# Kernel optimization log

Measured on AMD Instinct MI355X. Metric: run time of the kernel, lower is better.

Reference implementation:

```python
import jax, jax.numpy as jnp
import numpy as np

HID = 128          # hidden_channels
NG = 256           # number of graphs in batch
NL = 50000         # ligand nodes
NP = 150000        # protein nodes
E = 500000         # edges (ligand->protein); rev edges are the reverse
RBF_COUNT = 8
D_MAX = 5.0


def _rbf(d):
    # d: [E] distances -> [E, 8] gaussian RBF expansion (D_min=0, D_max=5, count=8)
    mu = jnp.linspace(0.0, D_MAX, RBF_COUNT)
    sigma = D_MAX / RBF_COUNT
    return jnp.exp(-(((d[:, None] - mu[None, :]) / sigma) ** 2))


def setup_inputs() -> dict:
    key = jax.random.key(0)
    ks = jax.random.split(key, 24)
    s = 0.05
    inp = {
        "x_ligand": jax.random.normal(ks[0], (NL, 44), jnp.float32),
        "x_protein": jax.random.normal(ks[1], (NP, 44), jnp.float32),
        "edge_attr": jax.random.uniform(ks[2], (E, 1), jnp.float32) * D_MAX,
        "edge_src": jax.random.randint(ks[3], (E,), 0, NL),
        "edge_dst": jax.random.randint(ks[4], (E,), 0, NP),
        "ligand_batch": jnp.sort(jax.random.randint(ks[5], (NL,), 0, NG)),
        # shared node embedding and edge embedding
        "W_node": jax.random.normal(ks[6], (44, HID), jnp.float32) * s,
        "W_el": jax.random.normal(ks[7], (1, 8), jnp.float32) * s,
        # 6 NConvs: index = layer*2 + (0: ligand->protein, 1: protein->ligand)
        "Wb": jax.random.normal(ks[8], (6, RBF_COUNT, HID), jnp.float32) * s,
        "bb": jnp.zeros((6, HID), jnp.float32),
        "Wn": jax.random.normal(ks[9], (6, HID, HID), jnp.float32) * s,
        "Ws": jax.random.normal(ks[10], (6, HID, HID), jnp.float32) * s,
        "bconv": jnp.zeros((6, HID), jnp.float32),
        # edge MLP: [2*HID+8 -> 512 -> 128] (BN in eval mode = identity, dropout off)
        "W1": jax.random.normal(ks[11], (2 * HID + 8, 512), jnp.float32) * s,
        "b1": jnp.zeros((512,), jnp.float32),
        "W2": jax.random.normal(ks[12], (512, 128), jnp.float32) * s,
        "b2": jnp.zeros((128,), jnp.float32),
        # lin_mpl: 128 -> out_channels//2 = 128
        "Wm": jax.random.normal(ks[13], (128, 128), jnp.float32) * s,
        "bm": jnp.zeros((128,), jnp.float32),
    }
    return inp


def _nconv(x_src, x_dst, src, dst, n_dst, rbf_feat, Wb_i, bb_i, Wn_i, Ws_i, b_i):
    # base = SiLU(Linear(rbf)); message = fc_neigh(base * x_j); aggr = mean over dst
    base = jax.nn.silu(rbf_feat @ Wb_i + bb_i)              # [E, HID]
    msg = (base * x_src[src]) @ Wn_i                         # gather + mul + GEMM
    agg = jax.ops.segment_sum(msg, dst, num_segments=n_dst)  # [n_dst, HID]
    deg = jax.ops.segment_sum(jnp.ones((src.shape[0], 1), msg.dtype), dst,
                              num_segments=n_dst)
    agg = agg / jnp.maximum(deg, 1.0)
    return x_dst @ Ws_i + agg + b_i


def reference(x_ligand, x_protein, edge_attr, edge_src, edge_dst, ligand_batch,
              W_node, W_el, Wb, bb, Wn, Ws, bconv, W1, b1, W2, b2, Wm, bm):
    lrelu = lambda v: jax.nn.leaky_relu(v, 0.01)
    xl = x_ligand @ W_node   # [NL, HID]
    xp = x_protein @ W_node  # [NP, HID]
    rbf_feat = _rbf(jnp.squeeze(edge_attr, -1))  # [E, 8]

    xl_sum = jnp.zeros_like(xl)
    xp_sum = jnp.zeros_like(xp)
    for l in range(3):
        i_lp, i_pl = 2 * l, 2 * l + 1
        # HeteroConv applies both edge types to the SAME input dict
        xp_new = lrelu(_nconv(xl, xp, edge_src, edge_dst, NP, rbf_feat,
                              Wb[i_lp], bb[i_lp], Wn[i_lp], Ws[i_lp], bconv[i_lp]))
        xl_new = lrelu(_nconv(xp, xl, edge_dst, edge_src, NL, rbf_feat,
                              Wb[i_pl], bb[i_pl], Wn[i_pl], Ws[i_pl], bconv[i_pl]))
        xl, xp = xl_new, xp_new
        xl_sum = xl_sum + xl
        xp_sum = xp_sum + xp

    # edge readout on the ligand->protein edges
    edge_repr = jnp.concatenate([xl_sum[edge_src], xp_sum[edge_dst]], axis=-1)
    d_pl = edge_attr @ W_el                                   # [E, 8]
    edge_repr = jnp.concatenate([edge_repr, d_pl], axis=1)    # [E, 2*HID+8]
    # edge_mlp (eval mode: BatchNorm identity, dropout off)
    m_pl = jax.nn.relu(edge_repr @ W1 + b1) @ W2 + b2         # [E, 128]
    w_pl = jnp.tanh(m_pl @ Wm + bm)                           # [E, 128]
    edge_batch = ligand_batch[edge_src]
    m_w = jax.ops.segment_sum(w_pl * m_pl, edge_batch, num_segments=NG)
    m_max = jax.ops.segment_max(m_pl, edge_batch, num_segments=NG)
    m_max = jnp.where(jnp.isfinite(m_max), m_max, 0.0)        # empty segments -> 0
    return jnp.concatenate([m_w, m_max], axis=1)              # [NG, 256]
```

## Files before the change

kernel.cpp:

```cpp
#include <hip/hip_runtime.h>
#include <hip/hip_bf16.h>


#define NLn 50000
#define NPn 150000
#define En  500000
#define NBL 1563
#define NBP 4688

typedef __attribute__((ext_vector_type(8))) short short8;
typedef __attribute__((ext_vector_type(4))) float float4v;

__device__ __forceinline__ float bf2f(unsigned short u){ return __uint_as_float(((unsigned)u) << 16); }
__device__ __forceinline__ float bflo(unsigned u){ return __uint_as_float(u << 16); }
__device__ __forceinline__ float bfhi(unsigned u){ return __uint_as_float(u & 0xffff0000u); }
__device__ __forceinline__ unsigned short f2bf(float f){
  __hip_bfloat16 h = __float2bfloat16(f);
  return *reinterpret_cast<unsigned short*>(&h);
}
__device__ __forceinline__ unsigned encf(float f){
  unsigned u = __float_as_uint(f);
  return (u & 0x80000000u) ? ~u : (u | 0x80000000u);
}
__device__ __forceinline__ float tanh_fast(float x){
  return 1.f - 2.f/(__expf(2.f*x) + 1.f);
}

__global__ __launch_bounds__(256) void k_embed(
    const float* __restrict__ Xl, const float* __restrict__ Xp,
    const float* __restrict__ Wnode,
    unsigned short* __restrict__ xl0, unsigned short* __restrict__ xp0){
  __shared__ float xs[1408];
  int b = blockIdx.x, tid = threadIdx.x;
  bool isL = b < NBL;
  const float* X = isL ? Xl : Xp;
  unsigned short* out = isL ? xl0 : xp0;
  int n = isL ? NLn : NPn;
  int n0 = (isL ? b : b - NBL) * 32;
  int nrows = n - n0; if (nrows > 32) nrows = 32;
  int nflt = nrows * 44;
  const float4* Xv = (const float4*)(X + (size_t)n0*44);
  for (int j = tid; j*4 < nflt; j += 256){
    float4 v = Xv[j];
    xs[j*4+0]=v.x; xs[j*4+1]=v.y; xs[j*4+2]=v.z; xs[j*4+3]=v.w;
  }
  __syncthreads();
  int c = tid & 127, half = tid >> 7;
  float acc[16];
  #pragma unroll
  for (int r=0;r<16;r++) acc[r]=0.f;
  const float* xrow = xs + half*16*44;
  #pragma unroll 4
  for (int k=0;k<44;k++){
    float w = Wnode[k*128 + c];
    #pragma unroll
    for (int r=0;r<16;r++) acc[r] += xrow[r*44 + k] * w;
  }
  int rbase = n0 + half*16;
  #pragma unroll
  for (int r=0;r<16;r++){
    int nn = rbase + r;
    if (nn < n) out[(size_t)nn*128 + c] = f2bf(acc[r]);
  }
}

__global__ __launch_bounds__(256) void k_prep(
    unsigned* __restrict__ cntz, unsigned* __restrict__ mmaxz, unsigned* __restrict__ outz,
    const float* __restrict__ Wel, const float* __restrict__ W1, float* __restrict__ vvec,
    const float* __restrict__ W2, unsigned short* __restrict__ w2t,
    const float* __restrict__ Wm, unsigned short* __restrict__ wmt,
    const float* __restrict__ Ws, const float* __restrict__ Wn,
    unsigned short* __restrict__ wcat, unsigned short* __restrict__ w1t,
    const float* __restrict__ Wb, const float* __restrict__ bb,
    unsigned short* __restrict__ lut){
  __shared__ float gw[16];
  int b = blockIdx.x, tid = threadIdx.x;
  if (b < 196){
    for (long i = (long)b*256 + tid; i < 200000; i += 196*256) cntz[i] = 0u;
  } else if (b < 324){
    mmaxz[(b-196)*256 + tid] = 0u;
  } else if (b < 580){
    outz[(b-324)*256 + tid] = 0u;
  } else if (b < 582){
    int j = (b-580)*256 + tid;
    float s = 0.f;
    #pragma unroll
    for (int r=0;r<8;r++) s += Wel[r]*W1[(256+r)*512 + j];
    vvec[j] = s;
  } else if (b < 838){
    int gid = (b-582)*256 + tid;
    int n = gid >> 9, k = gid & 511;
    w2t[n*512 + k] = f2bf(W2[k*128 + n]);
  } else if (b < 902){
    int gid = (b-838)*256 + tid;
    int n = gid >> 7, k = gid & 127;
    wmt[n*128 + k] = f2bf(Wm[k*128 + n]);
  } else if (b < 1670){
    int gid = (b-902)*256 + tid;
    int i = gid >> 15, rem = gid & 32767;
    int n = rem >> 8, k = rem & 255;
    float v = (k < 128) ? Ws[i*16384 + k*128 + n] : Wn[i*16384 + (k-128)*128 + n];
    wcat[gid] = f2bf(v);
  } else if (b < 2182){
    int gid = (b-1670)*256 + tid;
    int part = gid >> 16, rem = gid & 65535;
    int n = rem >> 7, k = rem & 127;
    w1t[gid] = f2bf(W1[(part*128 + k)*512 + n]);
  } else {
    int gid0 = (b-2182)*256;
    int c = tid & 127, half = tid >> 7;
    int bin0 = (gid0 >> 7) & 4095;
    int i = gid0 >> 19;
    if (tid < 16){
      int bn = bin0 + (tid >> 3), j = tid & 7;
      float d = ((float)bn + 0.5f) * 0.001220703125f;
      float a = (d - 0.7142857143f*(float)j) * 1.6f;
      gw[tid] = __expf(-a*a);
    }
    __syncthreads();
    float s = bb[i*128 + c];
    const float* g = gw + half*8;
    #pragma unroll
    for (int j=0;j<8;j++) s += g[j] * Wb[i*1024 + j*128 + c];
    lut[gid0 + tid] = f2bf(s / (1.f + __expf(-s)));
  }
}

__global__ __launch_bounds__(256) void k_count(const int* __restrict__ esrc,
    const int* __restrict__ edst, unsigned* __restrict__ cntL, unsigned* __restrict__ cntP){
  int e = blockIdx.x*256 + threadIdx.x;
  if (e >= En) return;
  atomicAdd(&cntL[esrc[e]], 1u);
  atomicAdd(&cntP[edst[e]], 1u);
}
__global__ __launch_bounds__(256) void k_cs2(const unsigned* __restrict__ cntL,
    unsigned* __restrict__ rowptrL, unsigned* __restrict__ bsumL,
    const unsigned* __restrict__ cntP, unsigned* __restrict__ rowptrP,
    unsigned* __restrict__ bsumP){
  bool isL = blockIdx.x < 49;
  const unsigned* cnt = isL ? cntL : cntP;
  unsigned* rowptr = isL ? rowptrL : rowptrP;
  unsigned* bsum = isL ? bsumL : bsumP;
  int n = isL ? NLn : NPn;
  int lb = isL ? blockIdx.x : blockIdx.x - 49;
  __shared__ unsigned ts[256];
  int tid = threadIdx.x;
  int base = lb*1024 + tid*4;
  unsigned v[4], run = 0;
  #pragma unroll
  for (int j=0;j<4;j++){ v[j] = run; run += (base+j < n) ? cnt[base+j] : 0u; }
  ts[tid] = run; __syncthreads();
  for (int off=1; off<256; off<<=1){
    unsigned t = (tid>=off) ? ts[tid-off] : 0u; __syncthreads();
    ts[tid] += t; __syncthreads();
  }
  unsigned excl = ts[tid] - run;
  #pragma unroll
  for (int j=0;j<4;j++) if (base+j < n) rowptr[base+j] = excl + v[j];
  if (tid == 255) bsum[lb] = ts[255];
}
__global__ void k_sb2(unsigned* __restrict__ bsumL, unsigned* __restrict__ bsumP){
  unsigned* bsum = blockIdx.x ? bsumP : bsumL;
  int nc = blockIdx.x ? 147 : 49;
  __shared__ unsigned ts[256];
  int tid = threadIdx.x;
  unsigned x = (tid < nc) ? bsum[tid] : 0u;
  ts[tid] = x; __syncthreads();
  for (int off=1; off<256; off<<=1){
    unsigned t = (tid>=off) ? ts[tid-off] : 0u; __syncthreads();
    ts[tid] += t; __syncthreads();
  }
  if (tid < nc) bsum[tid] = ts[tid] - x;
}
__global__ __launch_bounds__(256) void k_ao2(
    unsigned* __restrict__ rowptrL, unsigned* __restrict__ cursorL,
    const unsigned* __restrict__ bsumL,
    unsigned* __restrict__ rowptrP, unsigned* __restrict__ cursorP,
    const unsigned* __restrict__ bsumP){
  bool isL = blockIdx.x < 196;
  unsigned* rowptr = isL ? rowptrL : rowptrP;
  unsigned* cursor = isL ? cursorL : cursorP;
  const unsigned* bsum = isL ? bsumL : bsumP;
  int n = isL ? NLn : NPn;
  int i = (isL ? blockIdx.x : blockIdx.x - 196)*256 + threadIdx.x;
  if (i < n){
    unsigned r = rowptr[i] + bsum[i>>10];
    rowptr[i] = r; cursor[i] = r;
  }
  if (i == 0) rowptr[n] = En;
}
__global__ __launch_bounds__(256) void k_place(const int* __restrict__ esrc,
    const int* __restrict__ edst, const float* __restrict__ ea,
    const int* __restrict__ lbatch, unsigned* __restrict__ curL,
    unsigned* __restrict__ curP, uint4* __restrict__ edgeL,
    int* __restrict__ idxL, int* __restrict__ idxP){
  int e = blockIdx.x*256 + threadIdx.x;
  if (e >= En) return;
  int s = esrc[e], d = edst[e];
  float dd = ea[e];
  int bin = (int)(dd * 819.2f);
  bin = (bin < 0) ? 0 : ((bin > 4095) ? 4095 : bin);
  unsigned pl = atomicAdd(&curL[s], 1u);
  uint4 er; er.x = (unsigned)s; er.y = (unsigned)d;
  er.z = __float_as_uint(dd); er.w = (unsigned)lbatch[s];
  edgeL[pl] = er;
  idxL[pl] = d | (bin << 18);
  unsigned pp = atomicAdd(&curP[d], 1u);
  idxP[pp] = s | (bin << 18);
}

#define EDGE_CAP 1024
__global__ __launch_bounds__(512, 8) void k_conv2(
    const unsigned short* __restrict__ xp_in, const unsigned short* __restrict__ xl_in,
    unsigned short* __restrict__ xp_out, unsigned short* __restrict__ xl_out,
    unsigned short* __restrict__ xp_sum, unsigned short* __restrict__ xl_sum,
    const unsigned* __restrict__ rowptrP, const int* __restrict__ idxP,
    const unsigned* __restrict__ rowptrL, const int* __restrict__ idxL,
    const unsigned short* __restrict__ lut_lp,
    const unsigned short* __restrict__ wcat_lp, const float* __restrict__ bias_lp,
    const unsigned short* __restrict__ lut_pl,
    const unsigned short* __restrict__ wcat_pl, const float* __restrict__ bias_pl,
    int first){
  __shared__ unsigned short ab[32][264];
  __shared__ unsigned short ob[32][136];
  __shared__ int snb[EDGE_CAP];
  __shared__ unsigned rps[33];
  int tid = threadIdx.x;
  int c2 = tid & 63, grp = tid >> 6;
  int bid = blockIdx.x;
  bool isP; int pb;
  if ((bid & 3) == 3){ isP = false; pb = bid >> 2; }
  else if (bid == 6250){ isP = false; pb = 1562; }
  else { isP = true; pb = (bid >> 2)*3 + (bid & 3); }
  const unsigned short* xdst_in = isP ? xp_in : xl_in;
  const unsigned short* xsrc_in = isP ? xl_in : xp_in;
  unsigned short* xout = isP ? xp_out : xl_out;
  unsigned short* xsum = isP ? xp_sum : xl_sum;
  const unsigned* rowptr = isP ? rowptrP : rowptrL;
  const int* eidx = isP ? idxP : idxL;
  const unsigned short* lut_i = isP ? lut_lp : lut_pl;
  const unsigned short* wcat = isP ? wcat_lp : wcat_pl;
  const float* bias = isP ? bias_lp : bias_pl;
  int ndst = isP ? NPn : NLn;
  int n0 = pb * 32;

  if (tid < 33){
    int idx = n0 + tid; if (idx > ndst) idx = ndst;
    rps[tid] = rowptr[idx];
  }
  __syncthreads();
  int r00 = (int)rps[0], rEnd = (int)rps[32];
  int eblk = rEnd - r00;
  bool fits = (eblk <= EDGE_CAP);
  if (fits){
    for (int p = tid; p < eblk; p += 512) snb[p] = eidx[r00 + p];
  }
  __syncthreads();

  const unsigned short* lutc = lut_i + 2*c2;
  const unsigned short* xc = xsrc_in + 2*c2;
  for (int m = grp*4; m < grp*4+4; m++){
    int n = n0 + m;
    float al0=0.f,ah0=0.f,al1=0.f,ah1=0.f,al2=0.f,ah2=0.f,al3=0.f,ah3=0.f;
    int dg = 1;
    if (n < ndst){
      *(unsigned*)&ab[m][2*c2] = *(const unsigned*)&xdst_in[(size_t)n*128 + 2*c2];
      int r0 = (int)rps[m], r1 = (int)rps[m+1];
      dg = r1 - r0;
      int p = r0;
      for (; p + 7 < r1; p += 8){
        int v[8];
        #pragma unroll
        for (int j=0;j<8;j++) v[j] = fits ? snb[p-r00+j] : eidx[p+j];
        unsigned lv[8], xv[8];
        #pragma unroll
        for (int j=0;j<8;j++){
          lv[j] = *(const unsigned*)&lutc[(size_t)((unsigned)v[j] >> 18)*128];
          xv[j] = *(const unsigned*)&xc[(size_t)(v[j] & 0x3FFFF)*128];
        }
        #pragma unroll
        for (int j=0;j<8;j++){
          switch (j & 3){
            case 0: al0 += bflo(lv[j])*bflo(xv[j]); ah0 += bfhi(lv[j])*bfhi(xv[j]); break;
            case 1: al1 += bflo(lv[j])*bflo(xv[j]); ah1 += bfhi(lv[j])*bfhi(xv[j]); break;
            case 2: al2 += bflo(lv[j])*bflo(xv[j]); ah2 += bfhi(lv[j])*bfhi(xv[j]); break;
            default: al3 += bflo(lv[j])*bflo(xv[j]); ah3 += bfhi(lv[j])*bfhi(xv[j]); break;
          }
        }
      }
      for (; p + 3 < r1; p += 4){
        int v0,v1,v2,v3;
        if (fits){
          v0 = snb[p-r00]; v1 = snb[p-r00+1]; v2 = snb[p-r00+2]; v3 = snb[p-r00+3];
        } else {
          v0 = eidx[p]; v1 = eidx[p+1]; v2 = eidx[p+2]; v3 = eidx[p+3];
        }
        unsigned l0 = *(const unsigned*)&lutc[(size_t)((unsigned)v0 >> 18)*128];
        unsigned x0 = *(const unsigned*)&xc[(size_t)(v0 & 0x3FFFF)*128];
        unsigned l1 = *(const unsigned*)&lutc[(size_t)((unsigned)v1 >> 18)*128];
        unsigned x1 = *(const unsigned*)&xc[(size_t)(v1 & 0x3FFFF)*128];
        unsigned l2 = *(const unsigned*)&lutc[(size_t)((unsigned)v2 >> 18)*128];
        unsigned x2 = *(const unsigned*)&xc[(size_t)(v2 & 0x3FFFF)*128];
        unsigned l3 = *(const unsigned*)&lutc[(size_t)((unsigned)v3 >> 18)*128];
        unsigned x3 = *(const unsigned*)&xc[(size_t)(v3 & 0x3FFFF)*128];
        al0 += bflo(l0)*bflo(x0); ah0 += bfhi(l0)*bfhi(x0);
        al1 += bflo(l1)*bflo(x1); ah1 += bfhi(l1)*bfhi(x1);
        al2 += bflo(l2)*bflo(x2); ah2 += bfhi(l2)*bfhi(x2);
        al3 += bflo(l3)*bflo(x3); ah3 += bfhi(l3)*bfhi(x3);
      }
      for (; p < r1; p++){
        int v0 = fits ? snb[p-r00] : eidx[p];
        unsigned l0 = *(const unsigned*)&lutc[(size_t)((unsigned)v0 >> 18)*128];
        unsigned x0 = *(const unsigned*)&xc[(size_t)(v0 & 0x3FFFF)*128];
        al0 += bflo(l0)*bflo(x0); ah0 += bfhi(l0)*bfhi(x0);
      }
    } else {
      *(unsigned*)&ab[m][2*c2] = 0u;
    }
    float inv = 1.f / (float)(dg > 1 ? dg : 1);
    float alo = ((al0+al1)+(al2+al3)) * inv;
    float ahi = ((ah0+ah1)+(ah2+ah3)) * inv;
    *(unsigned*)&ab[m][128 + 2*c2] = (unsigned)f2bf(alo) | ((unsigned)f2bf(ahi) << 16);
  }
  __syncthreads();

  int wave = tid >> 6, lane = tid & 63, quad = lane >> 4, l15 = lane & 15;
  int mt = wave & 1, nh = wave >> 1;
  int arow = mt*16 + l15;
  float4v acc[2] = {{0,0,0,0},{0,0,0,0}};
  for (int k0 = 0; k0 < 256; k0 += 32){
    short8 A = *(const short8*)&ab[arow][k0 + quad*8];
    #pragma unroll
    for (int nt=0;nt<2;nt++){
      short8 B = *(const short8*)&wcat[(size_t)(nh*32 + nt*16 + l15)*256 + k0 + quad*8];
      acc[nt] = __builtin_amdgcn_mfma_f32_16x16x32_bf16(A, B, acc[nt], 0, 0, 0);
    }
  }
  #pragma unroll
  for (int nt=0;nt<2;nt++){
    int col = nh*32 + nt*16 + l15;
    float bc = bias[col];
    #pragma unroll
    for (int r=0;r<4;r++){
      int row = mt*16 + quad*4 + r;
      float v = acc[nt][r] + bc;
      ob[row][col] = f2bf((v > 0.f) ? v : 0.01f*v);
    }
  }
  __syncthreads();
  for (int m = grp*4; m < grp*4+4; m++){
    int n = n0 + m;
    if (n < ndst){
      unsigned vb = *(unsigned*)&ob[m][2*c2];
      size_t off = (size_t)n*128 + 2*c2;
      *(unsigned*)&xout[off] = vb;
      if (first){
        *(unsigned*)&xsum[off] = vb;
      } else {
        unsigned so = *(unsigned*)&xsum[off];
        float lo = bflo(so) + bflo(vb);
        float hi = bfhi(so) + bfhi(vb);
        *(unsigned*)&xsum[off] = (unsigned)f2bf(lo) | ((unsigned)f2bf(hi) << 16);
      }
    }
  }
}

__global__ __launch_bounds__(512) void k_hproj3(
    const unsigned short* __restrict__ xl_s, const unsigned short* __restrict__ xp_s,
    const unsigned short* __restrict__ w1t, const float* __restrict__ b1,
    unsigned* __restrict__ h_l, unsigned* __restrict__ h_p){
  __shared__ unsigned short hb[32][528];
  int tid = threadIdx.x, lane = tid & 63, wave = tid >> 6;
  int quad = lane >> 4, l15 = lane & 15;
  bool isL = blockIdx.x < 256;
  const unsigned short* xs = isL ? xl_s : xp_s;
  const unsigned short* wt = isL ? w1t : w1t + 65536;
  unsigned* hout = isL ? h_l : h_p;
  int nn = isL ? NLn : NPn;
  int ntile = isL ? NBL : NBP;
  int wg = isL ? blockIdx.x : blockIdx.x - 256;
  int stride = isL ? 256 : 768;

  short8 Bk[4][4];
  float bv[4];
  #pragma unroll
  for (int nt=0;nt<4;nt++){
    int row = wave*64 + nt*16 + l15;
    #pragma unroll
    for (int kk=0;kk<4;kk++)
      Bk[nt][kk] = *(const short8*)&wt[(size_t)row*128 + kk*32 + quad*8];
    bv[nt] = isL ? b1[row] : 0.f;
  }

  for (int t = wg; t < ntile; t += stride){
    int n0 = t*32;
    int a0r = n0 + l15;      if (a0r >= nn) a0r = nn-1;
    int a1r = n0 + 16 + l15; if (a1r >= nn) a1r = nn-1;
    float4v acc[2][4];
    #pragma unroll
    for (int m2=0;m2<2;m2++)
      #pragma unroll
      for (int nt=0;nt<4;nt++) acc[m2][nt] = (float4v){0,0,0,0};
    #pragma unroll
    for (int kk=0;kk<4;kk++){
      short8 A0 = *(const short8*)&xs[(size_t)a0r*128 + kk*32 + quad*8];
      short8 A1 = *(const short8*)&xs[(size_t)a1r*128 + kk*32 + quad*8];
      #pragma unroll
      for (int nt=0;nt<4;nt++){
        acc[0][nt] = __builtin_amdgcn_mfma_f32_16x16x32_bf16(A0, Bk[nt][kk], acc[0][nt], 0, 0, 0);
        acc[1][nt] = __builtin_amdgcn_mfma_f32_16x16x32_bf16(A1, Bk[nt][kk], acc[1][nt], 0, 0, 0);
      }
    }
    #pragma unroll
    for (int m2=0;m2<2;m2++){
      #pragma unroll
      for (int nt=0;nt<4;nt++){
        int col = wave*64 + nt*16 + l15;
        #pragma unroll
        for (int r=0;r<4;r++)
          hb[m2*16 + quad*4 + r][col] = f2bf(acc[m2][nt][r] + bv[nt]);
      }
    }
    __syncthreads();
    for (int idx = tid; idx < 8192; idx += 512){
      int m = idx >> 8, d = idx & 255;
      int n = n0 + m;
      if (n < nn){
        unsigned pack = (unsigned)hb[m][2*d] | ((unsigned)hb[m][2*d+1] << 16);
        hout[(size_t)n*256 + d] = pack;
      }
    }
    __syncthreads();
  }
}

__global__ __launch_bounds__(512) void k_readout4(
    const unsigned* __restrict__ hl, const unsigned* __restrict__ hp,
    const uint4* __restrict__ edgeL, const float* __restrict__ vvec,
    const unsigned short* __restrict__ w2t, const float* __restrict__ b2,
    const unsigned short* __restrict__ wmt, const float* __restrict__ bm,
    float* __restrict__ outw, unsigned* __restrict__ mmax){
  __shared__ __align__(16) unsigned short lds[37120];
  unsigned short (*msb)[136] = (unsigned short(*)[136])(lds + 32768);
  int tid = threadIdx.x, lane = tid & 63, wave = tid >> 6;
  int quad = lane >> 4, l15 = lane & 15;
  int ns = wave*16;

  int wg = (blockIdx.x & 7)*128 + (blockIdx.x >> 3);
  int nt_tot = En/32;
  int t0 = wg*16;
  int t1 = t0 + 16; if (t1 > nt_tot) t1 = nt_tot;
  if (t0 >= t1) return;

  short8 Bk[16];
  #pragma unroll
  for (int kk=0;kk<16;kk++)
    Bk[kk] = *(const short8*)&w2t[(size_t)(ns + l15)*512 + kk*32 + quad*8];
  short8 Bm[4];
  #pragma unroll
  for (int kk=0;kk<4;kk++)
    Bm[kk] = *(const short8*)&wmt[(size_t)(ns + l15)*128 + kk*32 + quad*8];
  float b2c0 = b2[ns + l15];
  float bm0  = bm[ns + l15];

  float4v vva = *(const float4v*)&vvec[lane*8];
  float4v vvb = *(const float4v*)&vvec[lane*8 + 4];
  int sw = lane & 31;
  const uint4* hl4 = (const uint4*)hl;
  const uint4* hp4 = (const uint4*)hp;
  const unsigned* e32 = (const unsigned*)edgeL;

  int si_prev = -1;
  uint4 ua = {0,0,0,0};
  int lm = wave*16 + (lane & 15);
  int le = lane & 31;

  #define H_EDGE(UA, UB, DD, I, WB)                                          \
    {                                                                        \
      unsigned o0,o1,o2,o3; float hx,hy;                                     \
      hx = fmaxf(bflo(UA.x)+bflo(UB.x)+(DD)*vva.x, 0.f);                     \
      hy = fmaxf(bfhi(UA.x)+bfhi(UB.x)+(DD)*vva.y, 0.f);                     \
      o0 = (unsigned)f2bf(hx) | ((unsigned)f2bf(hy) << 16);                  \
      hx = fmaxf(bflo(UA.y)+bflo(UB.y)+(DD)*vva.z, 0.f);                     \
      hy = fmaxf(bfhi(UA.y)+bfhi(UB.y)+(DD)*vva.w, 0.f);                     \
      o1 = (unsigned)f2bf(hx) | ((unsigned)f2bf(hy) << 16);                  \
      hx = fmaxf(bflo(UA.z)+bflo(UB.z)+(DD)*vvb.x, 0.f);                     \
      hy = fmaxf(bfhi(UA.z)+bfhi(UB.z)+(DD)*vvb.y, 0.f);                     \
      o2 = (unsigned)f2bf(hx) | ((unsigned)f2bf(hy) << 16);                  \
      hx = fmaxf(bflo(UA.w)+bflo(UB.w)+(DD)*vvb.z, 0.f);                     \
      hy = fmaxf(bfhi(UA.w)+bfhi(UB.w)+(DD)*vvb.w, 0.f);                     \
      o3 = (unsigned)f2bf(hx) | ((unsigned)f2bf(hy) << 16);                  \
      uint4 ov; ov.x=o0; ov.y=o1; ov.z=o2; ov.w=o3;                          \
      *(uint4*)&lds[(WB) + lane*256 + (((I) ^ sw) << 3)] = ov;               \
    }

  unsigned md1 = 0; int br_cur = 0, br1 = 0;
  {
    unsigned md0 = e32[(size_t)t0*128 + lm];
    br_cur = (int)e32[((size_t)(t0*32 + le))*4 + 3];
    #pragma unroll
    for (int ii=0; ii<4; ii++){
      int si = __builtin_amdgcn_readfirstlane(__shfl((int)md0, ii*4));
      int di = __builtin_amdgcn_readfirstlane(__shfl((int)md0, ii*4 + 1));
      float dd = __uint_as_float((unsigned)__builtin_amdgcn_readfirstlane(__shfl((int)md0, ii*4 + 2)));
      if (si != si_prev){ ua = hl4[(size_t)si*64 + lane]; si_prev = si; }
      uint4 ub = hp4[(size_t)di*64 + lane];
      H_EDGE(ua, ub, dd, wave*4 + ii, 0)
    }
    if (t0 + 1 < t1){
      md1 = e32[(size_t)(t0+1)*128 + lm];
      br1 = (int)e32[((size_t)((t0+1)*32 + le))*4 + 3];
    }
    __syncthreads();
  }

  int cur = 0;
  unsigned md2 = md1; int br2 = br1;
  for (int t = t0; t < t1; ++t){
    bool pf = (t + 1 < t1);
    if (t + 2 < t1){
      md2 = e32[(size_t)(t+2)*128 + lm];
      br2 = (int)e32[((size_t)((t+2)*32 + le))*4 + 3];
    }
    uint4 ub0, ub1, ub2, ub3;
    if (pf){
      int d0 = __builtin_amdgcn_readfirstlane(__shfl((int)md1, 1));
      int d1 = __builtin_amdgcn_readfirstlane(__shfl((int)md1, 5));
      int d2 = __builtin_amdgcn_readfirstlane(__shfl((int)md1, 9));
      int d3 = __builtin_amdgcn_readfirstlane(__shfl((int)md1, 13));
      ub0 = hp4[(size_t)d0*64 + lane];
      ub1 = hp4[(size_t)d1*64 + lane];
      ub2 = hp4[(size_t)d2*64 + lane];
      ub3 = hp4[(size_t)d3*64 + lane];
      int s0 = __builtin_amdgcn_readfirstlane(__shfl((int)md1, 0));
      if (s0 != si_prev){ ua = hl4[(size_t)s0*64 + lane]; si_prev = s0; }
    }

    int rb = cur ? 16384 : 0;
    float4v acc[2] = {{0,0,0,0},{0,0,0,0}};
    #pragma unroll
    for (int kk = 0; kk < 16; kk++){
      int kcc = kk*4 + quad;
      int sw2 = kcc & 31;
      short8 A0 = *(const short8*)&lds[rb + kcc*256 + ((l15 ^ sw2) << 3)];
      short8 A1 = *(const short8*)&lds[rb + kcc*256 + (((16 + l15) ^ sw2) << 3)];
      acc[0] = __builtin_amdgcn_mfma_f32_16x16x32_bf16(A0, Bk[kk], acc[0], 0, 0, 0);
      acc[1] = __builtin_amdgcn_mfma_f32_16x16x32_bf16(A1, Bk[kk], acc[1], 0, 0, 0);
    }
    float mreg[2][4];
    #pragma unroll
    for (int mt=0;mt<2;mt++){
      int col = ns + l15;
      #pragma unroll
      for (int r=0;r<4;r++){
        float mv = acc[mt][r] + b2c0;
        mreg[mt][r] = mv;
        msb[mt*16 + quad*4 + r][col] = f2bf(mv);
      }
    }
    __syncthreads();

    float4v acc2[2] = {{0,0,0,0},{0,0,0,0}};
    #pragma unroll
    for (int kk = 0; kk < 4; kk++){
      short8 A0 = *(const short8*)&msb[l15][kk*32 + quad*8];
      short8 A1 = *(const short8*)&msb[16 + l15][kk*32 + quad*8];
      acc2[0] = __builtin_amdgcn_mfma_f32_16x16x32_bf16(A0, Bm[kk], acc2[0], 0, 0, 0);
      acc2[1] = __builtin_amdgcn_mfma_f32_16x16x32_bf16(A1, Bm[kk], acc2[1], 0, 0, 0);
    }
    {
      int b0 = __shfl(br_cur, 0);
      bool uni = (b0 == __shfl(br_cur, 31));
      int col = ns + l15;
      if (uni){
        float s = 0.f, mx = -3.402823466e38f;
        #pragma unroll
        for (int mt=0;mt<2;mt++){
          #pragma unroll
          for (int r=0;r<4;r++){
            float mv = mreg[mt][r];
            float tt = tanh_fast(acc2[mt][r] + bm0);
            s += tt*mv; mx = fmaxf(mx, mv);
          }
        }
        s += __shfl_xor(s, 16); s += __shfl_xor(s, 32);
        mx = fmaxf(mx, __shfl_xor(mx, 16)); mx = fmaxf(mx, __shfl_xor(mx, 32));
        if (quad == 0){
          atomicAdd(&outw[b0*256 + col], s);
          atomicMax(&mmax[b0*128 + col], encf(mx));
        }
      } else {
        #pragma unroll
        for (int mt=0;mt<2;mt++){
          #pragma unroll
          for (int r=0;r<4;r++){
            int row = mt*16 + quad*4 + r;
            int b = __shfl(br_cur, row);
            float mv = mreg[mt][r];
            float tt = tanh_fast(acc2[mt][r] + bm0);
            atomicAdd(&outw[b*256 + col], tt*mv);
            atomicMax(&mmax[b*128 + col], encf(mv));
          }
        }
      }
    }

    if (pf){
      int wb = cur ? 0 : 16384;
      #pragma unroll
      for (int ii=0; ii<4; ii++){
        int si = __builtin_amdgcn_readfirstlane(__shfl((int)md1, ii*4));
        float dd = __uint_as_float((unsigned)__builtin_amdgcn_readfirstlane(__shfl((int)md1, ii*4 + 2)));
        if (si != si_prev){ ua = hl4[(size_t)si*64 + lane]; si_prev = si; }
        uint4 ub = (ii==0) ? ub0 : (ii==1) ? ub1 : (ii==2) ? ub2 : ub3;
        H_EDGE(ua, ub, dd, wave*4 + ii, wb)
      }
    }
    __syncthreads();

    md1 = md2; br_cur = br1; br1 = br2;
    cur ^= 1;
  }
  #undef H_EDGE
}

__global__ __launch_bounds__(256) void k_final(const unsigned* __restrict__ mmax,
    float* __restrict__ out){
  int gid = blockIdx.x*256 + threadIdx.x;
  unsigned enc = mmax[gid];
  float v;
  if (enc == 0u) v = 0.f;
  else if (enc & 0x80000000u) v = __uint_as_float(enc & 0x7FFFFFFFu);
  else v = __uint_as_float(~enc);
  int g = gid >> 7, cc = gid & 127;
  out[g*256 + 128 + cc] = v;
}

extern "C" void kernel_launch(void* const* d_in, const int* in_sizes, int n_in,
                              void* d_out, int out_size, void* d_ws, size_t ws_size,
                              hipStream_t stream) {
  const float* x_l    = (const float*)d_in[0];
  const float* x_p    = (const float*)d_in[1];
  const float* ea     = (const float*)d_in[2];
  const int*   esrc   = (const int*)d_in[3];
  const int*   edst   = (const int*)d_in[4];
  const int*   lbatch = (const int*)d_in[5];
  const float* W_node = (const float*)d_in[6];
  const float* W_el   = (const float*)d_in[7];
  const float* Wb     = (const float*)d_in[8];
  const float* bb     = (const float*)d_in[9];
  const float* Wn     = (const float*)d_in[10];
  const float* Ws     = (const float*)d_in[11];
  const float* bconv  = (const float*)d_in[12];
  const float* W1     = (const float*)d_in[13];
  const float* b1     = (const float*)d_in[14];
  const float* W2     = (const float*)d_in[15];
  const float* b2     = (const float*)d_in[16];
  const float* Wm     = (const float*)d_in[17];
  const float* bm     = (const float*)d_in[18];

  char* w = (char*)d_ws;
  unsigned short* xl0 = (unsigned short*)(w + 0);
  unsigned short* xl1 = (unsigned short*)(w + 12800000);
  unsigned short* xp0 = (unsigned short*)(w + 25600000);
  unsigned short* xp1 = (unsigned short*)(w + 64000000);
  int*      idxP  = (int*)(w + 102400000);
  int*      idxL  = (int*)(w + 104400000);
  unsigned short* lut = (unsigned short*)(w + 106400000);
  unsigned* h_l   = (unsigned*)(w + 0);
  unsigned* h_p   = (unsigned*)(w + 51200000);
  unsigned short* xl_s = (unsigned short*)(w + 204800000);
  unsigned short* xp_s = (unsigned short*)(w + 217600000);
  unsigned short* wcat = (unsigned short*)(w + 256000000);
  unsigned short* w1t  = (unsigned short*)(w + 256393216);
  unsigned short* w2t  = (unsigned short*)(w + 256655360);
  unsigned short* wmt  = (unsigned short*)(w + 256786432);
  float*    vvec  = (float*)(w + 256819200);
  unsigned* mmax  = (unsigned*)(w + 256821248);
  unsigned* bsumL = (unsigned*)(w + 256952320);
  unsigned* bsumP = (unsigned*)(w + 256953344);
  unsigned* rowptrL = (unsigned*)(w + 256954368);
  unsigned* cursorL = (unsigned*)(w + 257154432);
  unsigned* rowptrP = (unsigned*)(w + 257354432);
  unsigned* cursorP = (unsigned*)(w + 257954496);
  unsigned* cntL    = (unsigned*)(w + 258554496);
  unsigned* cntP    = (unsigned*)(w + 258754496);
  uint4*    edgeL   = (uint4*)(w + 259354496);

  float* out = (float*)d_out;

  k_prep<<<14470, 256, 0, stream>>>(
      (unsigned*)(w + 258554496), mmax, (unsigned*)d_out,
      W_el, W1, vvec, W2, w2t, Wm, wmt, Ws, Wn, wcat, w1t, Wb, bb, lut);
  k_embed<<<NBL + NBP, 256, 0, stream>>>(x_l, x_p, W_node, xl0, xp0);

  k_count<<<1954, 256, 0, stream>>>(esrc, edst, cntL, cntP);
  k_cs2<<<196, 256, 0, stream>>>(cntL, rowptrL, bsumL, cntP, rowptrP, bsumP);
  k_sb2<<<2, 256, 0, stream>>>(bsumL, bsumP);
  k_ao2<<<782, 256, 0, stream>>>(rowptrL, cursorL, bsumL, rowptrP, cursorP, bsumP);
  k_place<<<1954, 256, 0, stream>>>(esrc, edst, ea, lbatch, cursorL, cursorP,
                                    edgeL, idxL, idxP);

  unsigned short *xlc = xl0, *xln = xl1, *xpc = xp0, *xpn = xp1;
  for (int l = 0; l < 3; ++l){
    int ilp = 2*l, ipl = 2*l + 1;
    k_conv2<<<NBP + NBL, 512, 0, stream>>>(
        xpc, xlc, xpn, xln, xp_s, xl_s,
        rowptrP, idxP, rowptrL, idxL,
        lut + (size_t)ilp*524288, wcat + ilp*32768, bconv + ilp*128,
        lut + (size_t)ipl*524288, wcat + ipl*32768, bconv + ipl*128,
        (l == 0) ? 1 : 0);
    unsigned short* t;
    t = xlc; xlc = xln; xln = t;
    t = xpc; xpc = xpn; xpn = t;
  }

  k_hproj3<<<1024, 512, 0, stream>>>(xl_s, xp_s, w1t, b1, h_l, h_p);

  k_readout4<<<1024, 512, 0, stream>>>(h_l, h_p, edgeL, vvec,
                                       w2t, b2, wmt, bm, out, mmax);
  k_final<<<128, 256, 0, stream>>>(mmax, out);
}
```

Before: 1.095 ms.

## Accumulate segment partials in registers across tiles and raise MFMA wave priority

Per-tile sum and max partials are now carried in registers while consecutive edge tiles fall in the same graph segment. The atomicAdd/atomicMax pair is issued only when the segment changes or the loop ends, which cuts global atomic traffic per tile. s_setprio is also raised around the MFMA loops to favour matrix-issuing waves. Edges are grouped by ligand, so consecutive tiles usually share a graph and the flush should be rare; the risk is extra register pressure.

```diff
diff --git a/kernel.cpp b/kernel.cpp
--- a/kernel.cpp
+++ b/kernel.cpp
@@ -463,6 +463,7 @@
     Bm[kk] = *(const short8*)&wmt[(size_t)(ns + l15)*128 + kk*32 + quad*8];
   float b2c0 = b2[ns + l15];
   float bm0  = bm[ns + l15];
+  int col = ns + l15;
 
   float4v vva = *(const float4v*)&vvec[lane*8];
   float4v vvb = *(const float4v*)&vvec[lane*8 + 4];
@@ -475,6 +476,9 @@
   uint4 ua = {0,0,0,0};
   int lm = wave*16 + (lane & 15);
   int le = lane & 31;
+
+  float sacc = 0.f, mxacc = -3.402823466e38f;
+  int cur_b = -1;
 
   #define H_EDGE(UA, UB, DD, I, WB)                                          \
     {                                                                        \
@@ -495,6 +499,18 @@
       *(uint4*)&lds[(WB) + lane*256 + (((I) ^ sw) << 3)] = ov;               \
     }
 
+  #define FLUSH_ACC()                                                        \
+    {                                                                        \
+      float fs = sacc, fx = mxacc;                                           \
+      fs += __shfl_xor(fs, 16); fs += __shfl_xor(fs, 32);                    \
+      fx = fmaxf(fx, __shfl_xor(fx, 16)); fx = fmaxf(fx, __shfl_xor(fx, 32));\
+      if (quad == 0){                                                        \
+        atomicAdd(&outw[cur_b*256 + col], fs);                               \
+        atomicMax(&mmax[cur_b*128 + col], encf(fx));                         \
+      }                                                                      \
+      sacc = 0.f; mxacc = -3.402823466e38f;                                  \
+    }
+
   unsigned md1 = 0; int br_cur = 0, br1 = 0;
   {
     unsigned md0 = e32[(size_t)t0*128 + lm];
@@ -539,6 +555,7 @@
 
     int rb = cur ? 16384 : 0;
     float4v acc[2] = {{0,0,0,0},{0,0,0,0}};
+    __builtin_amdgcn_s_setprio(1);
     #pragma unroll
     for (int kk = 0; kk < 16; kk++){
       int kcc = kk*4 + quad;
@@ -548,10 +565,10 @@
       acc[0] = __builtin_amdgcn_mfma_f32_16x16x32_bf16(A0, Bk[kk], acc[0], 0, 0, 0);
       acc[1] = __builtin_amdgcn_mfma_f32_16x16x32_bf16(A1, Bk[kk], acc[1], 0, 0, 0);
     }
+    __builtin_amdgcn_s_setprio(0);
     float mreg[2][4];
     #pragma unroll
     for (int mt=0;mt<2;mt++){
-      int col = ns + l15;
       #pragma unroll
       for (int r=0;r<4;r++){
         float mv = acc[mt][r] + b2c0;
@@ -562,6 +579,7 @@
     __syncthreads();
 
     float4v acc2[2] = {{0,0,0,0},{0,0,0,0}};
+    __builtin_amdgcn_s_setprio(1);
     #pragma unroll
     for (int kk = 0; kk < 4; kk++){
       short8 A0 = *(const short8*)&msb[l15][kk*32 + quad*8];
@@ -569,28 +587,26 @@
       acc2[0] = __builtin_amdgcn_mfma_f32_16x16x32_bf16(A0, Bm[kk], acc2[0], 0, 0, 0);
       acc2[1] = __builtin_amdgcn_mfma_f32_16x16x32_bf16(A1, Bm[kk], acc2[1], 0, 0, 0);
     }
+    __builtin_amdgcn_s_setprio(0);
     {
       int b0 = __shfl(br_cur, 0);
       bool uni = (b0 == __shfl(br_cur, 31));
-      int col = ns + l15;
       if (uni){
-        float s = 0.f, mx = -3.402823466e38f;
+        if (cur_b != b0){
+          if (cur_b >= 0) FLUSH_ACC()
+          cur_b = b0;
+        }
         #pragma unroll
         for (int mt=0;mt<2;mt++){
           #pragma unroll
           for (int r=0;r<4;r++){
             float mv = mreg[mt][r];
             float tt = tanh_fast(acc2[mt][r] + bm0);
-            s += tt*mv; mx = fmaxf(mx, mv);
+            sacc += tt*mv; mxacc = fmaxf(mxacc, mv);
           }
         }
-        s += __shfl_xor(s, 16); s += __shfl_xor(s, 32);
-        mx = fmaxf(mx, __shfl_xor(mx, 16)); mx = fmaxf(mx, __shfl_xor(mx, 32));
-        if (quad == 0){
-          atomicAdd(&outw[b0*256 + col], s);
-          atomicMax(&mmax[b0*128 + col], encf(mx));
-        }
       } else {
+        if (cur_b >= 0){ FLUSH_ACC() cur_b = -1; }
         #pragma unroll
         for (int mt=0;mt<2;mt++){
           #pragma unroll
@@ -622,6 +638,8 @@
     md1 = md2; br_cur = br1; br1 = br2;
     cur ^= 1;
   }
+  if (cur_b >= 0) FLUSH_ACC()
+  #undef FLUSH_ACC
   #undef H_EDGE
 }
 
```

Result: no change. 1.079 ms (-1.5%).
